# Optimization experiments

Measured on AMD Instinct MI355X. Metric: run time of the kernel, lower is better.

## Reference

```python
import jax, jax.numpy as jnp
import numpy as np

NEG_SLOPE = 0.01  # nn.LeakyReLU default

N = 100000
E = 1600000
D_IN = 128
D_OUT = 128


def setup_inputs() -> dict:
    key = jax.random.key(0)
    ks = jax.random.split(key, 8)
    features = jax.random.normal(ks[0], (N, D_IN), dtype=jnp.float32)
    adj_rows = jax.random.randint(ks[1], (E,), 0, N, dtype=jnp.int64)
    adj_cols = jax.random.randint(ks[2], (E,), 0, N, dtype=jnp.int64)
    adj_vals = jax.random.uniform(ks[3], (E,), dtype=jnp.float32)
    s1 = 1.0 / np.sqrt(D_IN)
    W1 = jax.random.uniform(ks[4], (D_IN, D_OUT), jnp.float32, -s1, s1)
    b1 = jax.random.uniform(ks[5], (D_OUT,), jnp.float32, -s1, s1)
    W2 = jax.random.uniform(ks[6], (D_IN, D_OUT), jnp.float32, -s1, s1)
    b2 = jax.random.uniform(ks[7], (D_OUT,), jnp.float32, -s1, s1)
    return {"features": features, "adj_rows": adj_rows, "adj_cols": adj_cols,
            "adj_vals": adj_vals, "W1": W1, "b1": b1, "W2": W2, "b2": b2}


def reference(features, adj_rows, adj_cols, adj_vals, W1, b1, W2, b2):
    # h_neigh = adj @ features  (COO SpMM via gather + segment_sum)
    msgs = adj_vals[:, None] * features[adj_cols]          # [E, D_IN]
    h_neigh = jax.ops.segment_sum(msgs, adj_rows, num_segments=features.shape[0])
    term1 = (features + h_neigh) @ W1 + b1                 # W1(features + h_neigh)
    term2 = (features * h_neigh) @ W2 + b2                 # W2(features * h_neigh)
    pre = term1 + term2
    return jnp.where(pre >= 0, pre, NEG_SLOPE * pre)       # leaky_relu
```

## Files before the change

### kernel.cpp

```cpp
#include <hip/hip_runtime.h>

#define D 128
#define BM 64

typedef short short8 __attribute__((ext_vector_type(8)));
typedef unsigned short ushort8_t __attribute__((ext_vector_type(8)));
typedef float f32x4 __attribute__((ext_vector_type(4)));

__device__ __forceinline__ unsigned short f2bf(float x) {
    unsigned u = __float_as_uint(x);
    unsigned r = (u + 0x7fffu + ((u >> 16) & 1u)) >> 16;
    return (unsigned short)r;
}
__device__ __forceinline__ float bf2f(unsigned short u) {
    return __uint_as_float(((unsigned)u) << 16);
}

__global__ __launch_bounds__(256) void prep_kernel(
    const float4* __restrict__ feat4, ushort4* __restrict__ fbf4, int nf4,
    const float* __restrict__ W1, const float* __restrict__ W2,
    unsigned short* __restrict__ WT,
    const int* __restrict__ rows, int* __restrict__ bcnt,
    int E, int nb, int epb)
{
    __shared__ int cnt[1024];
    const int t = threadIdx.x;
    const int b = blockIdx.x;
    for (int i = t; i < nb; i += 256) cnt[i] = 0;
    __syncthreads();

    int e0 = b * epb;
    int e1 = e0 + epb; if (e1 > E) e1 = E;
    for (int e = e0 + t; e < e1; e += 256) atomicAdd(&cnt[rows[e] >> 7], 1);

    for (int i = b * 256 + t; i < nf4; i += 256 * 256) {
        float4 v = feat4[i];
        fbf4[i] = make_ushort4(f2bf(v.x), f2bf(v.y), f2bf(v.z), f2bf(v.w));
    }

    if (b < 128) {
        int idx = b * 256 + t;
        int c = idx & 127;
        int k = idx >> 7;
        float w = (k < 128) ? W1[k * 128 + c] : W2[(k - 128) * 128 + c];
        WT[c * 256 + k] = f2bf(w);
    }

    __syncthreads();
    for (int i = t; i < nb; i += 256)
        if (cnt[i]) atomicAdd(&bcnt[i], cnt[i]);
}

__global__ __launch_bounds__(256) void fconv_kernel(
    const float4* __restrict__ feat4, ushort4* __restrict__ fbf4, int total)
{
    int i = blockIdx.x * 256 + threadIdx.x;
    if (i < total) {
        float4 v = feat4[i];
        fbf4[i] = make_ushort4(f2bf(v.x), f2bf(v.y), f2bf(v.z), f2bf(v.w));
    }
}

__global__ __launch_bounds__(256) void wconv_kernel(
    const float* __restrict__ W1, const float* __restrict__ W2,
    unsigned short* __restrict__ WT)
{
    int idx = blockIdx.x * 256 + threadIdx.x;
    int c = idx & 127;
    int k = idx >> 7;
    float w = (k < 128) ? W1[k * 128 + c] : W2[(k - 128) * 128 + c];
    WT[c * 256 + k] = f2bf(w);
}

__global__ __launch_bounds__(1024) void bucket_scan_kernel(
    const int* __restrict__ bcnt, int* __restrict__ bstart,
    int* __restrict__ bcur, int nb, int E)
{
    __shared__ int wsum[16];
    int tid = threadIdx.x, lane = tid & 63, wid = tid >> 6;
    int x = (tid < nb) ? bcnt[tid] : 0;
    int v = x;
    #pragma unroll
    for (int off = 1; off < 64; off <<= 1) {
        int y = __shfl_up(v, off, 64);
        if (lane >= off) v += y;
    }
    if (lane == 63) wsum[wid] = v;
    __syncthreads();
    if (wid == 0 && lane < 16) {
        int s = wsum[lane];
        #pragma unroll
        for (int off = 1; off < 16; off <<= 1) {
            int y = __shfl_up(s, off, 64);
            if (lane >= off) s += y;
        }
        wsum[lane] = s;
    }
    __syncthreads();
    int wexcl = wid ? wsum[wid - 1] : 0;
    int excl = wexcl + v - x;
    if (tid < nb) { bstart[tid] = excl; bcur[tid] = excl; }
    if (tid == 0) bstart[nb] = E;
}

__global__ __launch_bounds__(256) void bucket_scatter_kernel(
    const int* __restrict__ rows, const int* __restrict__ cols,
    const float* __restrict__ vals, int* __restrict__ bcur,
    uint2* __restrict__ bsedge, int E, int nb)
{
    __shared__ int cnt[1024];
    __shared__ int base[1024];
    int t = threadIdx.x;
    int e0 = blockIdx.x * 4096;
    for (int i = t; i < nb; i += 256) cnt[i] = 0;
    __syncthreads();
    #pragma unroll
    for (int q = 0; q < 16; ++q) {
        int e = e0 + t + q * 256;
        if (e < E) atomicAdd(&cnt[rows[e] >> 7], 1);
    }
    __syncthreads();
    for (int i = t; i < nb; i += 256) {
        int c = cnt[i];
        if (c) { base[i] = atomicAdd(&bcur[i], c); cnt[i] = 0; }
    }
    __syncthreads();
    #pragma unroll
    for (int q = 0; q < 16; ++q) {
        int e = e0 + t + q * 256;
        if (e < E) {
            int r = rows[e];
            int b = r >> 7;
            int pos = base[b] + atomicAdd(&cnt[b], 1);
            bsedge[pos] = make_uint2(((unsigned)(r & 127) << 17) | (unsigned)cols[e],
                                     __float_as_uint(vals[e]));
        }
    }
}

__global__ __launch_bounds__(256) void bucket_sort_kernel(
    const uint2* __restrict__ bsedge,
    const int* __restrict__ bstart,
    uint2* __restrict__ sedge,
    int* __restrict__ row_start,
    int N, int E)
{
    __shared__ int cnt[128];
    __shared__ int base[128];
    const int b = blockIdx.x;
    const int t = threadIdx.x;
    const int s = bstart[b], e = bstart[b + 1];
    if (t < 128) cnt[t] = 0;
    __syncthreads();
    for (int j = s + t; j < e; j += 256)
        atomicAdd(&cnt[bsedge[j].x >> 17], 1);
    __syncthreads();
    if (t < 64) {
        int c0 = cnt[2 * t], c1 = cnt[2 * t + 1];
        int pair = c0 + c1;
        int v = pair;
        #pragma unroll
        for (int off = 1; off < 64; off <<= 1) {
            int y = __shfl_up(v, off, 64);
            if (t >= off) v += y;
        }
        int excl = v - pair;
        base[2 * t]     = excl;
        base[2 * t + 1] = excl + c0;
        cnt[2 * t] = 0;
        cnt[2 * t + 1] = 0;
    }
    __syncthreads();
    const int r0 = b << 7;
    if (t < 128 && r0 + t < N) row_start[r0 + t] = s + base[t];
    if (b == 0 && t == 0) row_start[N] = E;
    for (int j = s + t; j < e; j += 256) {
        uint2 ed = bsedge[j];
        int rl = ed.x >> 17;
        int p = atomicAdd(&cnt[rl], 1);
        sedge[s + base[rl] + p] = make_uint2(ed.x & 0x1FFFFu, ed.y);
    }
}

__global__ __launch_bounds__(256) void spmm_gemm16_kernel(
    const ushort8_t* __restrict__ fbf8,
    const int* __restrict__ row_start,
    const uint2* __restrict__ sedge,
    const unsigned short* __restrict__ WT,
    const float* __restrict__ b1, const float* __restrict__ b2,
    float* __restrict__ out, int N)
{
    __shared__ __align__(16) unsigned char am_raw[16 * 512];

    const int tid = threadIdx.x;
    const int block0 = blockIdx.x * 16;
    const int rq = tid >> 4;
    const int l  = tid & 15;

    int row = block0 + rq;
    float acc[8] = {};
    float f[8] = {};
    if (row < N) {
        int s = row_start[row];
        int e = row_start[row + 1];
        int j = s;
        for (; j + 7 < e; j += 8) {
            uint2 ed[8];
            #pragma unroll
            for (int q = 0; q < 8; ++q) ed[q] = sedge[j + q];
            ushort8_t ff[8];
            #pragma unroll
            for (int q = 0; q < 8; ++q)
                ff[q] = fbf8[(size_t)ed[q].x * 16 + l];
            #pragma unroll
            for (int q = 0; q < 8; ++q) {
                float v = __uint_as_float(ed[q].y);
                #pragma unroll
                for (int p = 0; p < 8; ++p)
                    acc[p] = fmaf(v, bf2f(ff[q][p]), acc[p]);
            }
        }
        for (; j + 3 < e; j += 4) {
            uint2 e0 = sedge[j],     e1 = sedge[j + 1];
            uint2 e2 = sedge[j + 2], e3 = sedge[j + 3];
            ushort8_t f0 = fbf8[(size_t)e0.x * 16 + l];
            ushort8_t f1 = fbf8[(size_t)e1.x * 16 + l];
            ushort8_t f2 = fbf8[(size_t)e2.x * 16 + l];
            ushort8_t f3 = fbf8[(size_t)e3.x * 16 + l];
            float v0 = __uint_as_float(e0.y), v1 = __uint_as_float(e1.y);
            float v2 = __uint_as_float(e2.y), v3 = __uint_as_float(e3.y);
            #pragma unroll
            for (int p = 0; p < 8; ++p) {
                acc[p] = fmaf(v0, bf2f(f0[p]), acc[p]);
                acc[p] = fmaf(v1, bf2f(f1[p]), acc[p]);
                acc[p] = fmaf(v2, bf2f(f2[p]), acc[p]);
                acc[p] = fmaf(v3, bf2f(f3[p]), acc[p]);
            }
        }
        for (; j < e; ++j) {
            uint2 e0 = sedge[j];
            float v = __uint_as_float(e0.y);
            ushort8_t f0 = fbf8[(size_t)e0.x * 16 + l];
            #pragma unroll
            for (int p = 0; p < 8; ++p) acc[p] = fmaf(v, bf2f(f0[p]), acc[p]);
        }
        ushort8_t fown = fbf8[(size_t)row * 16 + l];
        #pragma unroll
        for (int p = 0; p < 8; ++p) f[p] = bf2f(fown[p]);
    }
    ushort8_t av, mv;
    #pragma unroll
    for (int q = 0; q < 8; ++q) {
        av[q] = f2bf(f[q] + acc[q]);
        mv[q] = f2bf(f[q] * acc[q]);
    }
    {
        int swz = (rq & 7) << 4;
        unsigned char* rowp = am_raw + rq * 512;
        *(ushort8_t*)(rowp + ((16 * l) ^ swz))       = av;
        *(ushort8_t*)(rowp + 256 + ((16 * l) ^ swz)) = mv;
    }
    __syncthreads();

    const int lane = tid & 63;
    const int w    = tid >> 6;
    const int l15  = lane & 15;
    const int lk   = lane >> 4;
    const int rswz = (l15 & 7) << 4;

    f32x4 gacc[2] = {};
    const char* WTc = (const char*)WT;
    const unsigned char* arow = am_raw + l15 * 512;

    #pragma unroll
    for (int ks = 0; ks < 8; ++ks) {
        int kbyte = ks * 64 + lk * 16;
        short8 a = *(const short8*)(arow + (kbyte ^ rswz));
        #pragma unroll
        for (int nc = 0; nc < 2; ++nc) {
            int col = w * 32 + nc * 16 + l15;
            short8 b = *(const short8*)(WTc + col * 512 + kbyte);
            gacc[nc] = __builtin_amdgcn_mfma_f32_16x16x32_bf16(a, b, gacc[nc], 0, 0, 0);
        }
    }

    #pragma unroll
    for (int nc = 0; nc < 2; ++nc) {
        int col = w * 32 + nc * 16 + l15;
        float bias = b1[col] + b2[col];
        int rbase = block0 + lk * 4;
        #pragma unroll
        for (int r = 0; r < 4; ++r) {
            int orow = rbase + r;
            if (orow < N) {
                float v = gacc[nc][r] + bias;
                out[orow * 128 + col] = (v >= 0.f) ? v : 0.01f * v;
            }
        }
    }
}

__global__ __launch_bounds__(256) void spmm_ab_kernel(
    const float4* __restrict__ feat4,
    const ushort8_t* __restrict__ fbf8,
    const int* __restrict__ row_start,
    const uint2* __restrict__ sedge,
    unsigned char* __restrict__ ambf, int N)
{
    int t = blockIdx.x * 256 + threadIdx.x;
    int row = t >> 4;
    int l   = t & 15;
    if (row >= N) return;

    int s = row_start[row];
    int e = row_start[row + 1];

    float acc[8] = {};
    int j = s;
    for (; j + 1 < e; j += 2) {
        uint2 e0 = sedge[j], e1 = sedge[j + 1];
        float v0 = __uint_as_float(e0.y), v1 = __uint_as_float(e1.y);
        ushort8_t f0 = fbf8[(size_t)e0.x * 16 + l];
        ushort8_t f1 = fbf8[(size_t)e1.x * 16 + l];
        #pragma unroll
        for (int q = 0; q < 8; ++q) {
            acc[q] = fmaf(v0, bf2f(f0[q]), acc[q]);
            acc[q] = fmaf(v1, bf2f(f1[q]), acc[q]);
        }
    }
    if (j < e) {
        uint2 e0 = sedge[j];
        float v = __uint_as_float(e0.y);
        ushort8_t f = fbf8[(size_t)e0.x * 16 + l];
        #pragma unroll
        for (int q = 0; q < 8; ++q) acc[q] = fmaf(v, bf2f(f[q]), acc[q]);
    }

    float4 fa = feat4[(size_t)row * 32 + 2 * l];
    float4 fb = feat4[(size_t)row * 32 + 2 * l + 1];
    float f[8] = { fa.x, fa.y, fa.z, fa.w, fb.x, fb.y, fb.z, fb.w };

    ushort8_t av, mv;
    #pragma unroll
    for (int q = 0; q < 8; ++q) {
        av[q] = f2bf(f[q] + acc[q]);
        mv[q] = f2bf(f[q] * acc[q]);
    }

    int swz = (row & 7) << 4;
    unsigned char* rowp = ambf + (size_t)row * 512;
    *(ushort8_t*)(rowp + ((16 * l) ^ swz))       = av;
    *(ushort8_t*)(rowp + 256 + ((16 * l) ^ swz)) = mv;
}

__global__ __launch_bounds__(256) void mfma_gemm2_kernel(
    const unsigned char* __restrict__ ambf,
    const unsigned short* __restrict__ WT,
    const float* __restrict__ b1, const float* __restrict__ b2,
    float* __restrict__ out, int N)
{
    __shared__ __align__(16) unsigned char am_raw[64 * 512];

    const int tid = threadIdx.x;
    const int block0 = blockIdx.x * BM;

    const short8* src = (const short8*)(ambf + (size_t)block0 * 512);
    short8* dst = (short8*)am_raw;
    #pragma unroll
    for (int it = 0; it < 8; ++it) {
        int idx = tid + it * 256;
        dst[idx] = src[idx];
    }
    __syncthreads();

    const int lane = tid & 63;
    const int w    = tid >> 6;
    const int wr   = w >> 1;
    const int wc   = w & 1;
    const int l15  = lane & 15;
    const int lk   = lane >> 4;
    const int rswz = (l15 & 7) << 4;

    f32x4 acc[2][4] = {};

    const char* WTc = (const char*)WT;
    const unsigned char* arow0 = am_raw + (wr * 32 + l15) * 512;
    const unsigned char* arow1 = arow0 + 16 * 512;

    #pragma unroll
    for (int ks = 0; ks < 8; ++ks) {
        int kbyte = ks * 64 + lk * 16;
        int akoff = kbyte ^ rswz;
        short8 a0 = *(const short8*)(arow0 + akoff);
        short8 a1 = *(const short8*)(arow1 + akoff);
        short8 bfr[4];
        #pragma unroll
        for (int nc = 0; nc < 4; ++nc) {
            int col = wc * 64 + nc * 16 + l15;
            bfr[nc] = *(const short8*)(WTc + col * 512 + kbyte);
        }
        #pragma unroll
        for (int nc = 0; nc < 4; ++nc) {
            acc[0][nc] = __builtin_amdgcn_mfma_f32_16x16x32_bf16(a0, bfr[nc], acc[0][nc], 0, 0, 0);
            acc[1][nc] = __builtin_amdgcn_mfma_f32_16x16x32_bf16(a1, bfr[nc], acc[1][nc], 0, 0, 0);
        }
    }

    #pragma unroll
    for (int nc = 0; nc < 4; ++nc) {
        int col = wc * 64 + nc * 16 + l15;
        float bias = b1[col] + b2[col];
        #pragma unroll
        for (int mr = 0; mr < 2; ++mr) {
            int rbase = block0 + wr * 32 + mr * 16 + lk * 4;
            #pragma unroll
            for (int r = 0; r < 4; ++r) {
                int row = rbase + r;
                if (row < N) {
                    float v = acc[mr][nc][r] + bias;
                    out[row * 128 + col] = (v >= 0.f) ? v : 0.01f * v;
                }
            }
        }
    }
}

__global__ __launch_bounds__(256) void hist_kernel(
    const int* __restrict__ rows, int* __restrict__ counts, int E)
{
    int e = blockIdx.x * 256 + threadIdx.x;
    if (e < E) atomicAdd(&counts[rows[e]], 1);
}

__global__ __launch_bounds__(256) void scan_pass1(
    const int* __restrict__ counts, int* __restrict__ btot, int N)
{
    int tid = threadIdx.x;
    int i = blockIdx.x * 1024 + tid * 4;
    int s = 0;
    if (i + 3 < N) {
        int4 v = *(const int4*)(counts + i);
        s = v.x + v.y + v.z + v.w;
    } else {
        for (int q = 0; q < 4; ++q) if (i + q < N) s += counts[i + q];
    }
    #pragma unroll
    for (int off = 32; off >= 1; off >>= 1) s += __shfl_down(s, off, 64);
    __shared__ int ws[4];
    if ((tid & 63) == 0) ws[tid >> 6] = s;
    __syncthreads();
    if (tid == 0) btot[blockIdx.x] = ws[0] + ws[1] + ws[2] + ws[3];
}

__global__ __launch_bounds__(1024) void scan_pass2(
    const int* __restrict__ btot, int* __restrict__ boff, int nb)
{
    __shared__ int wsum[16];
    int tid = threadIdx.x, lane = tid & 63, wid = tid >> 6;
    int x = (tid < nb) ? btot[tid] : 0;
    int v = x;
    #pragma unroll
    for (int off = 1; off < 64; off <<= 1) {
        int y = __shfl_up(v, off, 64);
        if (lane >= off) v += y;
    }
    if (lane == 63) wsum[wid] = v;
    __syncthreads();
    if (wid == 0 && lane < 16) {
        int s = wsum[lane];
        #pragma unroll
        for (int off = 1; off < 16; off <<= 1) {
            int y = __shfl_up(s, off, 64);
            if (lane >= off) s += y;
        }
        wsum[lane] = s;
    }
    __syncthreads();
    int wexcl = wid ? wsum[wid - 1] : 0;
    if (tid < nb) boff[tid] = wexcl + v - x;
}

__global__ __launch_bounds__(256) void scan_pass3(
    int* __restrict__ row_start, int* __restrict__ cursor,
    const int* __restrict__ boff, int N, int E)
{
    int tid = threadIdx.x;
    int base = blockIdx.x * 1024 + tid * 4;
    int c0 = 0, c1 = 0, c2 = 0, c3 = 0;
    if (base + 3 < N) {
        int4 v = *(const int4*)(row_start + base);
        c0 = v.x; c1 = v.y; c2 = v.z; c3 = v.w;
    } else {
        if (base + 0 < N) c0 = row_start[base + 0];
        if (base + 1 < N) c1 = row_start[base + 1];
        if (base + 2 < N) c2 = row_start[base + 2];
        if (base + 3 < N) c3 = row_start[base + 3];
    }
    int s0 = c0, s1 = s0 + c1, s2 = s1 + c2, s3 = s2 + c3;
    int lane = tid & 63, wid = tid >> 6;
    int v = s3;
    #pragma unroll
    for (int off = 1; off < 64; off <<= 1) {
        int y = __shfl_up(v, off, 64);
        if (lane >= off) v += y;
    }
    __shared__ int ws[4];
    if (lane == 63) ws[wid] = v;
    __syncthreads();
    int wexcl = 0;
    for (int q = 0; q < wid; ++q) wexcl += ws[q];
    int texcl = wexcl + (v - s3) + boff[blockIdx.x];
    int e0 = texcl, e1 = texcl + s0, e2 = texcl + s1, e3 = texcl + s2;
    if (base + 0 < N) { row_start[base + 0] = e0; cursor[base + 0] = e0; }
    if (base + 1 < N) { row_start[base + 1] = e1; cursor[base + 1] = e1; }
    if (base + 2 < N) { row_start[base + 2] = e2; cursor[base + 2] = e2; }
    if (base + 3 < N) { row_start[base + 3] = e3; cursor[base + 3] = e3; }
    if (blockIdx.x == 0 && tid == 0) row_start[N] = E;
}

__global__ __launch_bounds__(256) void scatter_sort_kernel(
    const int* __restrict__ rows, const int* __restrict__ cols,
    const float* __restrict__ vals, int* __restrict__ cursor,
    uint2* __restrict__ sedge, int E)
{
    int e = blockIdx.x * 256 + threadIdx.x;
    if (e < E) {
        int r = rows[e];
        int p = atomicAdd(&cursor[r], 1);
        sedge[p] = make_uint2((unsigned)cols[e], __float_as_uint(vals[e]));
    }
}

__global__ __launch_bounds__(256) void spmm_kernel(
    const float2* __restrict__ feat2,
    const int* __restrict__ row_start,
    const uint2* __restrict__ sedge,
    float2* __restrict__ h2, int N)
{
    int gw = (blockIdx.x * 256 + threadIdx.x) >> 6;
    int lane = threadIdx.x & 63;
    if (gw >= N) return;
    int s = row_start[gw];
    int e = row_start[gw + 1];
    float2 acc = make_float2(0.f, 0.f);
    int j = s;
    for (; j + 1 < e; j += 2) {
        uint2 e0 = sedge[j], e1 = sedge[j + 1];
        float v0 = __uint_as_float(e0.y), v1 = __uint_as_float(e1.y);
        float2 f0 = feat2[(size_t)e0.x * 64 + lane];
        float2 f1 = feat2[(size_t)e1.x * 64 + lane];
        acc.x = fmaf(v0, f0.x, acc.x);
        acc.y = fmaf(v0, f0.y, acc.y);
        acc.x = fmaf(v1, f1.x, acc.x);
        acc.y = fmaf(v1, f1.y, acc.y);
    }
    if (j < e) {
        uint2 e0 = sedge[j];
        float v = __uint_as_float(e0.y);
        float2 f = feat2[(size_t)e0.x * 64 + lane];
        acc.x = fmaf(v, f.x, acc.x);
        acc.y = fmaf(v, f.y, acc.y);
    }
    h2[(size_t)gw * 64 + lane] = acc;
}

__global__ __launch_bounds__(256) void mfma_gemm_kernel(
    const float4* __restrict__ feat4, const float4* __restrict__ h4,
    const unsigned short* __restrict__ WT,
    const float* __restrict__ b1, const float* __restrict__ b2,
    float* __restrict__ out, int N)
{
    __shared__ __align__(16) unsigned char am_raw[64 * 512];
    const int tid = threadIdx.x;
    const int block0 = blockIdx.x * BM;
    #pragma unroll
    for (int it = 0; it < 8; ++it) {
        int idx  = tid + it * 256;
        int node = idx >> 5;
        int p    = idx & 31;
        int g    = block0 + node;
        float4 fv = make_float4(0.f, 0.f, 0.f, 0.f);
        float4 hv = make_float4(0.f, 0.f, 0.f, 0.f);
        if (g < N) { fv = feat4[g * 32 + p]; hv = h4[g * 32 + p]; }
        ushort4 av = make_ushort4(f2bf(fv.x + hv.x), f2bf(fv.y + hv.y),
                                  f2bf(fv.z + hv.z), f2bf(fv.w + hv.w));
        ushort4 mv = make_ushort4(f2bf(fv.x * hv.x), f2bf(fv.y * hv.y),
                                  f2bf(fv.z * hv.z), f2bf(fv.w * hv.w));
        int swz = (node & 7) << 4;
        *(ushort4*)(am_raw + node * 512 + ((p * 8) ^ swz))       = av;
        *(ushort4*)(am_raw + node * 512 + ((256 + p * 8) ^ swz)) = mv;
    }
    __syncthreads();
    const int lane = tid & 63;
    const int w    = tid >> 6;
    const int wr   = w >> 1;
    const int wc   = w & 1;
    const int l15  = lane & 15;
    const int lk   = lane >> 4;
    const int rswz = (l15 & 7) << 4;
    f32x4 acc[2][4] = {};
    const char* WTc = (const char*)WT;
    const unsigned char* arow0 = am_raw + (wr * 32 + l15) * 512;
    const unsigned char* arow1 = arow0 + 16 * 512;
    #pragma unroll
    for (int ks = 0; ks < 8; ++ks) {
        int kbyte = ks * 64 + lk * 16;
        int akoff = kbyte ^ rswz;
        short8 a0 = *(const short8*)(arow0 + akoff);
        short8 a1 = *(const short8*)(arow1 + akoff);
        short8 bfr[4];
        #pragma unroll
        for (int nc = 0; nc < 4; ++nc) {
            int col = wc * 64 + nc * 16 + l15;
            bfr[nc] = *(const short8*)(WTc + col * 512 + kbyte);
        }
        #pragma unroll
        for (int nc = 0; nc < 4; ++nc) {
            acc[0][nc] = __builtin_amdgcn_mfma_f32_16x16x32_bf16(a0, bfr[nc], acc[0][nc], 0, 0, 0);
            acc[1][nc] = __builtin_amdgcn_mfma_f32_16x16x32_bf16(a1, bfr[nc], acc[1][nc], 0, 0, 0);
        }
    }
    #pragma unroll
    for (int nc = 0; nc < 4; ++nc) {
        int col = wc * 64 + nc * 16 + l15;
        float bias = b1[col] + b2[col];
        #pragma unroll
        for (int mr = 0; mr < 2; ++mr) {
            int rbase = block0 + wr * 32 + mr * 16 + lk * 4;
            #pragma unroll
            for (int r = 0; r < 4; ++r) {
                int row = rbase + r;
                if (row < N) {
                    float v = acc[mr][nc][r] + bias;
                    out[row * 128 + col] = (v >= 0.f) ? v : 0.01f * v;
                }
            }
        }
    }
}

__global__ __launch_bounds__(256) void edge_scatter_kernel(
    const float4* __restrict__ feat4, const int* __restrict__ rows,
    const int* __restrict__ cols, const float* __restrict__ vals,
    float* __restrict__ h, int E)
{
    int idx = blockIdx.x * 256 + threadIdx.x;
    if (idx >= E * 32) return;
    int e = idx >> 5;
    int p = idx & 31;
    int r = rows[e];
    int c = cols[e];
    float v = vals[e];
    float4 f = feat4[c * 32 + p];
    float* hr = h + (long long)r * D + p * 4;
    unsafeAtomicAdd(hr + 0, v * f.x);
    unsafeAtomicAdd(hr + 1, v * f.y);
    unsafeAtomicAdd(hr + 2, v * f.z);
    unsafeAtomicAdd(hr + 3, v * f.w);
}

__global__ __launch_bounds__(256) void fused_gemm_kernel(
    const float* __restrict__ feat, const float* __restrict__ h,
    const float* __restrict__ W1, const float* __restrict__ b1,
    const float* __restrict__ W2, const float* __restrict__ b2,
    float* __restrict__ out, int N)
{
    __shared__ float a_lds[BM][D];
    __shared__ float m_lds[BM][D];
    const int tid = threadIdx.x;
    const int block0 = blockIdx.x * BM;
    const float4* feat4 = (const float4*)feat;
    const float4* h4    = (const float4*)h;
    #pragma unroll
    for (int it = 0; it < 8; ++it) {
        int idx  = tid + it * 256;
        int node = idx >> 5;
        int p    = idx & 31;
        int gnode = block0 + node;
        float4 fv = make_float4(0.f, 0.f, 0.f, 0.f);
        float4 hv = make_float4(0.f, 0.f, 0.f, 0.f);
        if (gnode < N) { fv = feat4[gnode * 32 + p]; hv = h4[gnode * 32 + p]; }
        float4 av = make_float4(fv.x + hv.x, fv.y + hv.y, fv.z + hv.z, fv.w + hv.w);
        float4 mv = make_float4(fv.x * hv.x, fv.y * hv.y, fv.z * hv.z, fv.w * hv.w);
        *(float4*)&a_lds[node][p * 4] = av;
        *(float4*)&m_lds[node][p * 4] = mv;
    }
    __syncthreads();
    const int c = tid & 31;
    const int g = tid >> 5;
    float acc[8][4] = {};
    const float4* W1v = (const float4*)W1;
    const float4* W2v = (const float4*)W2;
    for (int k = 0; k < D; ++k) {
        float4 w1 = W1v[k * 32 + c];
        float4 w2 = W2v[k * 32 + c];
        #pragma unroll
        for (int t = 0; t < 8; ++t) {
            float av = a_lds[g + 8 * t][k];
            float mv = m_lds[g + 8 * t][k];
            acc[t][0] = fmaf(av, w1.x, fmaf(mv, w2.x, acc[t][0]));
            acc[t][1] = fmaf(av, w1.y, fmaf(mv, w2.y, acc[t][1]));
            acc[t][2] = fmaf(av, w1.z, fmaf(mv, w2.z, acc[t][2]));
            acc[t][3] = fmaf(av, w1.w, fmaf(mv, w2.w, acc[t][3]));
        }
    }
    float4 bb1 = ((const float4*)b1)[c];
    float4 bb2 = ((const float4*)b2)[c];
    const float bx = bb1.x + bb2.x, by = bb1.y + bb2.y;
    const float bz = bb1.z + bb2.z, bw = bb1.w + bb2.w;
    #pragma unroll
    for (int t = 0; t < 8; ++t) {
        int gnode = block0 + g + 8 * t;
        if (gnode >= N) continue;
        float4 o;
        o.x = acc[t][0] + bx; o.y = acc[t][1] + by;
        o.z = acc[t][2] + bz; o.w = acc[t][3] + bw;
        o.x = (o.x >= 0.f) ? o.x : 0.01f * o.x;
        o.y = (o.y >= 0.f) ? o.y : 0.01f * o.y;
        o.z = (o.z >= 0.f) ? o.z : 0.01f * o.z;
        o.w = (o.w >= 0.f) ? o.w : 0.01f * o.w;
        ((float4*)out)[gnode * 32 + c] = o;
    }
}

extern "C" void kernel_launch(void* const* d_in, const int* in_sizes, int n_in,
                              void* d_out, int out_size, void* d_ws, size_t ws_size,
                              hipStream_t stream) {
    const float* feat = (const float*)d_in[0];
    const int*   rows = (const int*)d_in[1];
    const int*   cols = (const int*)d_in[2];
    const float* vals = (const float*)d_in[3];
    const float* W1   = (const float*)d_in[4];
    const float* b1   = (const float*)d_in[5];
    const float* W2   = (const float*)d_in[6];
    const float* b2   = (const float*)d_in[7];

    const int N = in_sizes[0] / D;
    const int E = in_sizes[1];
    float* out = (float*)d_out;

    const int NBK  = (N + 127) >> 7;
    const int Npad = NBK << 7;

    size_t off = 0;
    unsigned short* featbf = (unsigned short*)d_ws;                off += (size_t)N * D * 2;
    off = (off + 15) & ~(size_t)15;
    uint2* sedge = (uint2*)((char*)d_ws + off);                    off += (size_t)E * 8;
    unsigned short* WT = (unsigned short*)((char*)d_ws + off);     off += 128 * 256 * 2;
    int* row_start = (int*)((char*)d_ws + off);                    off += (size_t)(N + 1) * 4;
    off = (off + 15) & ~(size_t)15;
    uint2* bsedge = (uint2*)((char*)d_ws + off);                   off += (size_t)E * 8;
    int* bcnt   = (int*)((char*)d_ws + off);                       off += (size_t)NBK * 4;
    int* bstart = (int*)((char*)d_ws + off);                       off += (size_t)(NBK + 1) * 4;
    int* bcur   = (int*)((char*)d_ws + off);                       off += (size_t)NBK * 4;
    size_t need1a = off;

    if (ws_size >= need1a && NBK <= 1024 && N <= (1 << 17)) {
        hipMemsetAsync(bcnt, 0, (size_t)NBK * sizeof(int), stream);
        int epb = (E + 255) / 256;
        prep_kernel<<<256, 256, 0, stream>>>(
            (const float4*)feat, (ushort4*)featbf, N * 32,
            W1, W2, WT, rows, bcnt, E, NBK, epb);
        bucket_scan_kernel<<<1, 1024, 0, stream>>>(bcnt, bstart, bcur, NBK, E);
        bucket_scatter_kernel<<<(E + 4095) / 4096, 256, 0, stream>>>(
            rows, cols, vals, bcur, bsedge, E, NBK);
        bucket_sort_kernel<<<NBK, 256, 0, stream>>>(
            bsedge, bstart, sedge, row_start, N, E);
        spmm_gemm16_kernel<<<(N + 15) / 16, 256, 0, stream>>>(
            (const ushort8_t*)featbf, row_start, sedge,
            WT, b1, b2, out, N);
        return;
    }

    const int NB = (N + 1023) / 1024;
    off = 0;
    unsigned char* ambf = (unsigned char*)d_ws;                    off += (size_t)Npad * 512;
    featbf = (unsigned short*)((char*)d_ws + off);                 off += (size_t)N * D * 2;
    off = (off + 15) & ~(size_t)15;
    sedge = (uint2*)((char*)d_ws + off);                           off += (size_t)E * 8;
    WT = (unsigned short*)((char*)d_ws + off);                     off += 128 * 256 * 2;
    row_start = (int*)((char*)d_ws + off);                         off += (size_t)(N + 1) * 4;
    off = (off + 15) & ~(size_t)15;
    int* cursor = (int*)((char*)d_ws + off);                       off += (size_t)N * 4;
    int* btot = (int*)((char*)d_ws + off);                         off += (size_t)NB * 4;
    int* boff = (int*)((char*)d_ws + off);                         off += (size_t)NB * 4;
    size_t need1b = off;

    if (ws_size >= need1b && NB <= 1024) {
        hipMemsetAsync(row_start, 0, (size_t)(N + 1) * sizeof(int), stream);
        fconv_kernel<<<(N * 32 + 255) / 256, 256, 0, stream>>>(
            (const float4*)feat, (ushort4*)featbf, N * 32);
        wconv_kernel<<<128, 256, 0, stream>>>(W1, W2, WT);
        hist_kernel<<<(E + 255) / 256, 256, 0, stream>>>(rows, row_start, E);
        scan_pass1<<<NB, 256, 0, stream>>>(row_start, btot, N);
        scan_pass2<<<1, 1024, 0, stream>>>(btot, boff, NB);
        scan_pass3<<<NB, 256, 0, stream>>>(row_start, cursor, boff, N, E);
        scatter_sort_kernel<<<(E + 255) / 256, 256, 0, stream>>>(
            rows, cols, vals, cursor, sedge, E);
        spmm_ab_kernel<<<(N * 16 + 255) / 256, 256, 0, stream>>>(
            (const float4*)feat, (const ushort8_t*)featbf, row_start, sedge,
            ambf, N);
        mfma_gemm2_kernel<<<(N + BM - 1) / BM, 256, 0, stream>>>(
            ambf, WT, b1, b2, out, N);
        return;
    }

    off = 0;
    float* h = (float*)d_ws;                           off += (size_t)N * D * 4;
    int* row_start2 = (int*)((char*)d_ws + off);       off += (size_t)(N + 1) * 4;
    int* cursor2    = (int*)((char*)d_ws + off);       off += (size_t)N * 4;
    off = (off + 15) & ~(size_t)15;
    uint2* sedge2   = (uint2*)((char*)d_ws + off);     off += (size_t)E * 8;
    off = (off + 15) & ~(size_t)15;
    unsigned short* WT2 = (unsigned short*)((char*)d_ws + off); off += 128 * 256 * 2;
    int* btot2 = (int*)((char*)d_ws + off);            off += (size_t)NB * 4;
    int* boff2 = (int*)((char*)d_ws + off);            off += (size_t)NB * 4;
    size_t need2 = off;

    if (ws_size >= need2 && NB <= 1024) {
        hipMemsetAsync(row_start2, 0, (size_t)(N + 1) * sizeof(int), stream);
        wconv_kernel<<<128, 256, 0, stream>>>(W1, W2, WT2);
        hist_kernel<<<(E + 255) / 256, 256, 0, stream>>>(rows, row_start2, E);
        scan_pass1<<<NB, 256, 0, stream>>>(row_start2, btot2, N);
        scan_pass2<<<1, 1024, 0, stream>>>(btot2, boff2, NB);
        scan_pass3<<<NB, 256, 0, stream>>>(row_start2, cursor2, boff2, N, E);
        scatter_sort_kernel<<<(E + 255) / 256, 256, 0, stream>>>(
            rows, cols, vals, cursor2, sedge2, E);
        spmm_kernel<<<(N * 64 + 255) / 256, 256, 0, stream>>>(
            (const float2*)feat, row_start2, sedge2, (float2*)h, N);
        mfma_gemm_kernel<<<(N + BM - 1) / BM, 256, 0, stream>>>(
            (const float4*)feat, (const float4*)h, WT2, b1, b2, out, N);
        return;
    }

    size_t hbytes = (size_t)N * D * sizeof(float);
    float* hh = (ws_size >= hbytes) ? (float*)d_ws : out;
    hipMemsetAsync(hh, 0, hbytes, stream);
    edge_scatter_kernel<<<((size_t)E * 32 + 255) / 256, 256, 0, stream>>>(
        (const float4*)feat, rows, cols, vals, hh, E);
    fused_gemm_kernel<<<(N + BM - 1) / BM, 256, 0, stream>>>(
        feat, hh, W1, b1, W2, b2, out, N);
}
```

Measured before the change: 182.9 us.

## Balance SpMM edges evenly across row-groups with shared-memory atomic accumulation

Instead of each 16-thread group processing one row's edges (load imbalance from varying degree), the block's combined edge range is split into equal chunks per group, with local row id kept in the edge's upper bits and partial sums flushed to a shared-memory accumulator via atomicAdd when the row changes. Edges for the block are staged in LDS (up to 512). This targets degree-induced imbalance across lanes, but adds LDS atomics, extra zeroing and a sync, and reduces the inner unroll from 8 to 4.

New measurement: 240.3 us. +31.4%, slower.

```diff
diff --git a/kernel.cpp b/kernel.cpp
--- a/kernel.cpp
+++ b/kernel.cpp
@@ -178,7 +178,7 @@
         uint2 ed = bsedge[j];
         int rl = ed.x >> 17;
         int p = atomicAdd(&cnt[rl], 1);
-        sedge[s + base[rl] + p] = make_uint2(ed.x & 0x1FFFFu, ed.y);
+        sedge[s + base[rl] + p] = ed;
     }
 }
 
@@ -191,72 +191,92 @@
     float* __restrict__ out, int N)
 {
     __shared__ __align__(16) unsigned char am_raw[16 * 512];
+    __shared__ float hacc[16 * 128];
+    __shared__ uint2 eL[512];
 
     const int tid = threadIdx.x;
     const int block0 = blockIdx.x * 16;
-    const int rq = tid >> 4;
-    const int l  = tid & 15;
-
-    int row = block0 + rq;
+    const int g = tid >> 4;
+    const int l = tid & 15;
+
+    {
+        float4* hz = (float4*)hacc;
+        hz[tid]       = make_float4(0.f, 0.f, 0.f, 0.f);
+        hz[tid + 256] = make_float4(0.f, 0.f, 0.f, 0.f);
+    }
+
+    const int S = row_start[block0];
+    int rend = block0 + 16; if (rend > N) rend = N;
+    const int Eend = row_start[rend];
+    const int M = Eend - S;
+
+    for (int i = tid; i < M && i < 512; i += 256) eL[i] = sedge[S + i];
+    __syncthreads();
+
+    const int chunk = (M + 15) >> 4;
+    int j0 = S + g * chunk;
+    int j1 = j0 + chunk; if (j1 > Eend) j1 = Eend;
+
     float acc[8] = {};
-    float f[8] = {};
-    if (row < N) {
-        int s = row_start[row];
-        int e = row_start[row + 1];
-        int j = s;
-        for (; j + 7 < e; j += 8) {
-            uint2 ed[8];
-            #pragma unroll
-            for (int q = 0; q < 8; ++q) ed[q] = sedge[j + q];
-            ushort8_t ff[8];
-            #pragma unroll
-            for (int q = 0; q < 8; ++q)
-                ff[q] = fbf8[(size_t)ed[q].x * 16 + l];
-            #pragma unroll
-            for (int q = 0; q < 8; ++q) {
+    int cur = -1;
+    for (int j = j0; j < j1; j += 4) {
+        int n = j1 - j; if (n > 4) n = 4;
+        uint2 ed[4];
+        #pragma unroll
+        for (int q = 0; q < 4; ++q) {
+            int idx = j + q;
+            ed[q] = (q < n) ? ((idx - S < 512) ? eL[idx - S] : sedge[idx])
+                            : make_uint2(0u, 0u);
+        }
+        ushort8_t ff[4];
+        #pragma unroll
+        for (int q = 0; q < 4; ++q)
+            if (q < n) ff[q] = fbf8[(size_t)(ed[q].x & 0x1FFFFu) * 16 + l];
+        #pragma unroll
+        for (int q = 0; q < 4; ++q) {
+            if (q < n) {
+                int rl = (ed[q].x >> 17) & 15;
+                if (rl != cur) {
+                    if (cur >= 0) {
+                        #pragma unroll
+                        for (int p = 0; p < 8; ++p)
+                            atomicAdd(&hacc[cur * 128 + l * 8 + p], acc[p]);
+                    }
+                    cur = rl;
+                    #pragma unroll
+                    for (int p = 0; p < 8; ++p) acc[p] = 0.f;
+                }
                 float v = __uint_as_float(ed[q].y);
                 #pragma unroll
                 for (int p = 0; p < 8; ++p)
                     acc[p] = fmaf(v, bf2f(ff[q][p]), acc[p]);
             }
         }
-        for (; j + 3 < e; j += 4) {
-            uint2 e0 = sedge[j],     e1 = sedge[j + 1];
-            uint2 e2 = sedge[j + 2], e3 = sedge[j + 3];
-            ushort8_t f0 = fbf8[(size_t)e0.x * 16 + l];
-            ushort8_t f1 = fbf8[(size_t)e1.x * 16 + l];
-            ushort8_t f2 = fbf8[(size_t)e2.x * 16 + l];
-            ushort8_t f3 = fbf8[(size_t)e3.x * 16 + l];
-            float v0 = __uint_as_float(e0.y), v1 = __uint_as_float(e1.y);
-            float v2 = __uint_as_float(e2.y), v3 = __uint_as_float(e3.y);
+    }
+    if (cur >= 0) {
+        #pragma unroll
+        for (int p = 0; p < 8; ++p)
+            atomicAdd(&hacc[cur * 128 + l * 8 + p], acc[p]);
+    }
+    __syncthreads();
+
+    {
+        int row = block0 + g;
+        float f[8] = {};
+        if (row < N) {
+            ushort8_t fown = fbf8[(size_t)row * 16 + l];
             #pragma unroll
-            for (int p = 0; p < 8; ++p) {
-                acc[p] = fmaf(v0, bf2f(f0[p]), acc[p]);
-                acc[p] = fmaf(v1, bf2f(f1[p]), acc[p]);
-                acc[p] = fmaf(v2, bf2f(f2[p]), acc[p]);
-                acc[p] = fmaf(v3, bf2f(f3[p]), acc[p]);
-            }
-        }
-        for (; j < e; ++j) {
-            uint2 e0 = sedge[j];
-            float v = __uint_as_float(e0.y);
-            ushort8_t f0 = fbf8[(size_t)e0.x * 16 + l];
-            #pragma unroll
-            for (int p = 0; p < 8; ++p) acc[p] = fmaf(v, bf2f(f0[p]), acc[p]);
-        }
-        ushort8_t fown = fbf8[(size_t)row * 16 + l];
-        #pragma unroll
-        for (int p = 0; p < 8; ++p) f[p] = bf2f(fown[p]);
-    }
-    ushort8_t av, mv;
-    #pragma unroll
-    for (int q = 0; q < 8; ++q) {
-        av[q] = f2bf(f[q] + acc[q]);
-        mv[q] = f2bf(f[q] * acc[q]);
-    }
-    {
-        int swz = (rq & 7) << 4;
-        unsigned char* rowp = am_raw + rq * 512;
+            for (int p = 0; p < 8; ++p) f[p] = bf2f(fown[p]);
+        }
+        ushort8_t av, mv;
+        #pragma unroll
+        for (int p = 0; p < 8; ++p) {
+            float h = hacc[g * 128 + l * 8 + p];
+            av[p] = f2bf(f[p] + h);
+            mv[p] = f2bf(f[p] * h);
+        }
+        int swz = (g & 7) << 4;
+        unsigned char* rowp = am_raw + g * 512;
         *(ushort8_t*)(rowp + ((16 * l) ^ swz))       = av;
         *(ushort8_t*)(rowp + 256 + ((16 * l) ^ swz)) = mv;
     }
```
